# Optimization experiments

Hardware: AMD Instinct MI355X
Metric: run time of the kernel (lower is better)

Reference implementation:

```python
import jax, jax.numpy as jnp
import numpy as np

EMB = 1024
HEADS = 8
SEQ = 4096
LN_EPS = 1e-5


def _layernorm(x, g, b):
    mu = jnp.mean(x, axis=-1, keepdims=True)
    var = jnp.mean(jnp.square(x - mu), axis=-1, keepdims=True)
    return (x - mu) * jax.lax.rsqrt(var + LN_EPS) * g + b


def setup_inputs() -> dict:
    key = jax.random.key(0)
    ks = jax.random.split(key, 12)
    s = 1.0 / np.sqrt(EMB)
    sz = 1.0 / np.sqrt(EMB * HEADS)
    return {
        "history": jax.random.normal(ks[0], (SEQ, EMB), jnp.float32),
        "embdding": jax.random.normal(ks[1], (SEQ, EMB), jnp.float32),
        # per-head Linear weights, torch layout [out, in], stacked over heads
        "Wq_w": jax.random.uniform(ks[2], (HEADS, EMB, EMB), jnp.float32, -s, s),
        "Wq_b": jax.random.uniform(ks[3], (HEADS, EMB), jnp.float32, -s, s),
        "Wk_w": jax.random.uniform(ks[4], (HEADS, EMB, EMB), jnp.float32, -s, s),
        "Wk_b": jax.random.uniform(ks[5], (HEADS, EMB), jnp.float32, -s, s),
        "Wv_w": jax.random.uniform(ks[6], (HEADS, EMB, EMB), jnp.float32, -s, s),
        "Wv_b": jax.random.uniform(ks[7], (HEADS, EMB), jnp.float32, -s, s),
        "Wz_w": jax.random.uniform(ks[8], (EMB, EMB * HEADS), jnp.float32, -sz, sz),
        "Wz_b": jax.random.uniform(ks[9], (EMB,), jnp.float32, -sz, sz),
        "ln1_g": jnp.ones((EMB,), jnp.float32),
        "ln1_b": jnp.zeros((EMB,), jnp.float32),
        "Wf_w": jax.random.uniform(ks[10], (EMB, EMB), jnp.float32, -s, s),
        "Wf_b": jax.random.uniform(ks[11], (EMB,), jnp.float32, -s, s),
        "ln2_g": jnp.ones((EMB,), jnp.float32),
        "ln2_b": jnp.zeros((EMB,), jnp.float32),
    }


def reference(history, embdding, Wq_w, Wq_b, Wk_w, Wk_b, Wv_w, Wv_b,
              Wz_w, Wz_b, ln1_g, ln1_b, Wf_w, Wf_b, ln2_g, ln2_b):
    S, E = embdding.shape
    H = Wq_w.shape[0]
    # per-head linears (torch: y = x @ W.T + b), batched over heads
    Q = jnp.einsum('se,hfe->hsf', embdding, Wq_w) + Wq_b[:, None, :]  # [H,S,E]
    K = jnp.einsum('se,hfe->hsf', embdding, Wk_w) + Wk_b[:, None, :]
    V = jnp.einsum('se,hfe->hsf', history, Wv_w) + Wv_b[:, None, :]
    # K^T @ Q -> [H, E, E], softmax over dim=1 of the 2D matrix == last axis here
    scores = jnp.einsum('hse,hsf->hef', K, Q) / jnp.sqrt(jnp.asarray(E, Q.dtype))
    A = jax.nn.softmax(scores, axis=-1)  # [H,E,E]
    Zh = jnp.einsum('hse,hef->hsf', V, A)  # [H,S,E]
    Z = jnp.transpose(Zh, (1, 0, 2)).reshape(S, H * E)  # cat(dim=1) in head order
    O = Z @ Wz_w.T + Wz_b  # [S,E]
    LN1 = _layernorm(O, ln1_g, ln1_b) + embdding
    FN = LN1 @ Wf_w.T + Wf_b
    LN2 = _layernorm(FN, ln2_g, ln2_b) + LN1
    return LN2
```

## Files before the change

kernel.cpp:

```cpp
#include <hip/hip_runtime.h>


constexpr int EMB = 1024;
constexpr int SEQ = 4096;
constexpr int NH  = 8;

using f32x4  = __attribute__((ext_vector_type(4))) float;
using bf16x8 = __attribute__((ext_vector_type(8))) __bf16;
using us8    = __attribute__((ext_vector_type(8))) unsigned short;
using us4    = __attribute__((ext_vector_type(4))) unsigned short;

#define GLOAD_LDS16(g, l) __builtin_amdgcn_global_load_lds(                 \
    (const __attribute__((address_space(1))) void*)(g),                     \
    (__attribute__((address_space(3))) void*)(l), 16, 0, 0)

__device__ inline unsigned short f2bf(float x) {
  unsigned int u = __float_as_uint(x);
  u += 0x7FFFu + ((u >> 16) & 1u);
  return (unsigned short)(u >> 16);
}
__device__ inline float bf2f(unsigned short h) {
  return __uint_as_float(((unsigned int)h) << 16);
}
__device__ inline f32x4 ntl4(const float* p) {
  return __builtin_nontemporal_load((const f32x4*)p);
}
__device__ inline us4 cvt4(f32x4 x) {
  us4 o; o[0] = f2bf(x[0]); o[1] = f2bf(x[1]); o[2] = f2bf(x[2]); o[3] = f2bf(x[3]);
  return o;
}

template <int MODE>
__device__ __attribute__((always_inline)) void gemm_body(
    unsigned short* lds, int wg,
    const unsigned short* A, const unsigned short* B, void* Cout,
    int K, int lda, int ldb, int ldc,
    long long aZ, long long bZ, long long cZ, int nx, int ny,
    const float* e0, const float* e1, const float* e2, const float* e3,
    float* mpart, float* spart) {
  const int bx = wg % nx;
  const int by = (wg / nx) % ny;
  const int z  = wg / (nx * ny);
  A += (size_t)z * aZ;
  B += (size_t)z * bZ;
  const int tid = threadIdx.x;
  const int lane = tid & 63, wid = tid >> 6;
  const int wm = wid >> 1, wn = wid & 1;
  const int row0 = bx * 64, col0 = by * 128;

  unsigned short* As = lds;
  unsigned short* Bs = lds + 64 * 64;

  f32x4 acc[2][4] = {};
  const int lrow = lane & 15, kg = lane >> 4;
  const int lr = lane >> 3;
  const int lc = (lane & 7) * 8;

  const int nt = K >> 6;
  for (int t = 0; t < nt; ++t) {
    const int k0 = t << 6;
#pragma unroll
    for (int c = 0; c < 2; ++c) {
      int chunk = wid * 2 + c;
      int r = chunk * 8 + lr;
      GLOAD_LDS16(A + (size_t)(row0 + r) * lda + k0 + lc, &As[chunk * 512]);
    }
#pragma unroll
    for (int c = 0; c < 4; ++c) {
      int chunk = wid * 4 + c;
      int r = chunk * 8 + lr;
      GLOAD_LDS16(B + (size_t)(col0 + r) * ldb + k0 + lc, &Bs[chunk * 512]);
    }
    __syncthreads();
#pragma unroll
    for (int ks = 0; ks < 2; ++ks) {
      bf16x8 a[2], b[4];
      int koff = ks * 32 + kg * 8;
#pragma unroll
      for (int i = 0; i < 2; ++i)
        a[i] = *(const bf16x8*)&As[(wm * 32 + i * 16 + lrow) * 64 + koff];
#pragma unroll
      for (int j = 0; j < 4; ++j)
        b[j] = *(const bf16x8*)&Bs[(wn * 64 + j * 16 + lrow) * 64 + koff];
#pragma unroll
      for (int i = 0; i < 2; ++i)
#pragma unroll
        for (int j = 0; j < 4; ++j)
          acc[i][j] = __builtin_amdgcn_mfma_f32_16x16x32_bf16(a[i], b[j], acc[i][j], 0, 0, 0);
    }
    __syncthreads();
  }

  const int rb = (lane >> 4) * 4, cc = lane & 15;
  unsigned short* Cs = lds;
#pragma unroll
  for (int i = 0; i < 2; ++i) {
#pragma unroll
    for (int j = 0; j < 4; ++j) {
#pragma unroll
      for (int r = 0; r < 4; ++r) {
        float val = acc[i][j][r];
        int mm = wm * 32 + i * 16 + rb + r;
        int nn = wn * 64 + j * 16 + cc;
        if (MODE == 4) {
          int m = row0 + mm, n = col0 + nn;
          float bq = e0[z * EMB + m], uu = e1[z * EMB + n];
          float bk = e2[z * EMB + n], vv = e3[z * EMB + m];
          val = (val + bq * (uu + (float)SEQ * bk) + vv * bk) * (1.0f / 32.0f);
        } else if (MODE == 5) {
          val += e0[col0 + nn];
        }
        Cs[mm * 128 + nn] = f2bf(val);
      }
    }
  }
  __syncthreads();
  unsigned short* Cg = (unsigned short*)Cout + (size_t)z * cZ;
#pragma unroll
  for (int p = 0; p < 4; ++p) {
    int idx = p * 256 + tid;
    int row = idx >> 4, col = (idx & 15) * 8;
    *(us8*)(Cg + (size_t)(row0 + row) * ldc + col0 + col) =
        *(const us8*)&Cs[row * 128 + col];
  }
  if (MODE == 4) {
    int colx = tid >> 1, half = tid & 1;
    float mx = -1e30f;
#pragma unroll 8
    for (int r = 0; r < 32; ++r)
      mx = fmaxf(mx, bf2f(Cs[(half * 32 + r) * 128 + colx]));
    mx = fmaxf(mx, __shfl_xor(mx, 1));
    float se = 0.f;
#pragma unroll 8
    for (int r = 0; r < 32; ++r)
      se += __expf(bf2f(Cs[(half * 32 + r) * 128 + colx]) - mx);
    se += __shfl_xor(se, 1);
    if (half == 0) {
      size_t soff = ((size_t)z * 16 + bx) * EMB + col0 + colx;
      mpart[soff] = mx;
      spart[soff] = se;
    }
  }
}

template <int MODE>
__global__ __launch_bounds__(256) void gemm_nt(const unsigned short* __restrict__ A,
                                               const unsigned short* __restrict__ B,
                                               void* __restrict__ Cout,
                                               int K, int lda, int ldb, int ldc,
                                               long long aZ, long long bZ, long long cZ,
                                               int nx, int ny,
                                               const float* __restrict__ e0,
                                               const float* __restrict__ e1,
                                               const float* __restrict__ e2,
                                               const float* __restrict__ e3,
                                               float* __restrict__ mpart,
                                               float* __restrict__ spart) {
  __shared__ __align__(16) unsigned short lds[(64 + 128) * 64];
  const int q = gridDim.x >> 3;
  const int wg = (blockIdx.x & 7) * q + (blockIdx.x >> 3);
  gemm_body<MODE>(lds, wg, A, B, Cout, K, lda, ldb, ldc, aZ, bZ, cZ, nx, ny,
                  e0, e1, e2, e3, mpart, spart);
}

__global__ __launch_bounds__(256) void colsum_xt_k(const float* __restrict__ emb,
                                                   const float* __restrict__ Wv,
                                                   float* __restrict__ part,
                                                   unsigned short* __restrict__ XT,
                                                   unsigned short* __restrict__ WvT) {
  __shared__ float tileT[64][65];
  const int b = blockIdx.x, tid = threadIdx.x;
  if (b < 128) {
    int e = (b & 3) * 256 + tid;
    int y = b >> 2;
    float s = 0.f;
    for (int r = y * 128; r < y * 128 + 128; ++r) s += emb[(size_t)r * EMB + e];
    part[y * EMB + e] = s;
    return;
  }
  const float* src; unsigned short* dst; int R, r0, c0;
  if (b < 1152) {
    int tb = b - 128;
    src = emb; dst = XT; R = SEQ;
    r0 = (tb >> 4) * 64; c0 = (tb & 15) * 64;
  } else {
    int t2 = b - 1152, z = t2 >> 8, tt = t2 & 255;
    src = Wv + (size_t)z * EMB * EMB; dst = WvT + (size_t)z * EMB * EMB;
    R = EMB;
    r0 = (tt >> 4) * 64; c0 = (tt & 15) * 64;
  }
  int tx = tid & 15, ty = tid >> 4;
#pragma unroll
  for (int p = 0; p < 4; ++p) {
    int ir = p * 16 + ty;
    f32x4 x = ntl4(src + (size_t)(r0 + ir) * EMB + c0 + tx * 4);
    tileT[tx * 4 + 0][ir] = x[0]; tileT[tx * 4 + 1][ir] = x[1];
    tileT[tx * 4 + 2][ir] = x[2]; tileT[tx * 4 + 3][ir] = x[3];
  }
  __syncthreads();
#pragma unroll
  for (int p = 0; p < 4; ++p) {
    int orow = p * 16 + ty;
    f32x4 x;
    x[0] = tileT[orow][tx * 4 + 0]; x[1] = tileT[orow][tx * 4 + 1];
    x[2] = tileT[orow][tx * 4 + 2]; x[3] = tileT[orow][tx * 4 + 3];
    *(us4*)(dst + (size_t)(c0 + orow) * R + r0 + tx * 4) = cvt4(x);
  }
}

__global__ __launch_bounds__(256) void colsum_red_k(const float* __restrict__ part,
                                                    float* __restrict__ xbar) {
  int e = blockIdx.x * 256 + threadIdx.x;
  float s = 0.f;
  for (int y = 0; y < 32; ++y) s += part[y * EMB + e];
  xbar[e] = s;
}

__global__ __launch_bounds__(256) void gram_cvt_k(
    const unsigned short* __restrict__ XT, unsigned short* __restrict__ Gp,
    const float* __restrict__ Wk, const float* __restrict__ Wq,
    const float* __restrict__ hist, const float* __restrict__ Wz,
    const float* __restrict__ Wf, const float* __restrict__ xbar,
    unsigned short* __restrict__ Wkb, unsigned short* __restrict__ Wqb,
    unsigned short* __restrict__ Yb, unsigned short* __restrict__ Wzb,
    unsigned short* __restrict__ Wfb,
    float* __restrict__ u, float* __restrict__ v) {
  __shared__ __align__(16) unsigned short smem[(64 + 128) * 64];
  const int tid = threadIdx.x;
  if (blockIdx.x < 1024) {
    const int wg = ((int)blockIdx.x & 7) * 128 + ((int)blockIdx.x >> 3);
    gemm_body<1>(smem, wg, XT, XT, Gp, 512, SEQ, SEQ, EMB,
                 512, 512, (long long)EMB * EMB, 16, 8,
                 nullptr, nullptr, nullptr, nullptr, nullptr, nullptr);
    return;
  }
  int c = blockIdx.x - 1024;
  if (c < 4096) {
    int gw = c * 4 + (tid >> 6);
    int lane = tid & 63;
    const float* src = (gw < 8192) ? Wk : Wq;
    unsigned short* dst = (gw < 8192) ? Wkb : Wqb;
    float* dot = (gw < 8192) ? u : v;
    int row = gw & 8191;
    const float* sr = src + (size_t)row * EMB;
    const float4* xb4 = (const float4*)xbar;
    unsigned short* dr = dst + (size_t)row * EMB;
    float s = 0.f;
#pragma unroll
    for (int j = 0; j < 4; ++j) {
      int idx = j * 64 + lane;
      f32x4 x = ntl4(sr + idx * 4);
      float4 xb = xb4[idx];
      *(us4*)(dr + idx * 4) = cvt4(x);
      s += x[0] * xb.x + x[1] * xb.y + x[2] * xb.z + x[3] * xb.w;
    }
#pragma unroll
    for (int off = 32; off; off >>= 1) s += __shfl_down(s, off);
    if (lane == 0) dot[row] = s;
  } else {
    size_t f0 = (size_t)(c - 4096) * 8192;
    const float* src; unsigned short* dst; size_t loc;
    if (f0 < 4194304ull) { src = hist; dst = Yb; loc = f0; }
    else if (f0 < 12582912ull) { src = Wz; dst = Wzb; loc = f0 - 4194304ull; }
    else { src = Wf; dst = Wfb; loc = f0 - 12582912ull; }
#pragma unroll
    for (int p = 0; p < 8; ++p) {
      int i = p * 256 + tid;
      f32x4 x = ntl4(src + loc + i * 4);
      *(us4*)(dst + loc + i * 4) = cvt4(x);
    }
  }
}

__global__ __launch_bounds__(256) void mp_dvec_k(
    const unsigned short* __restrict__ Cbf, const unsigned short* __restrict__ Wzb,
    unsigned short* __restrict__ Mp,
    const float* __restrict__ bz, const float* __restrict__ cvec,
    float* __restrict__ d) {
  __shared__ __align__(16) unsigned short smem[(64 + 128) * 64];
  const int tid = threadIdx.x;
  if (blockIdx.x < 1024) {
    const int wg = ((int)blockIdx.x & 7) * 128 + ((int)blockIdx.x >> 3);
    gemm_body<1>(smem, wg, Cbf, Wzb, Mp, EMB, EMB, NH * EMB, EMB,
                 (long long)EMB * EMB, (long long)EMB, (long long)EMB * EMB, 16, 8,
                 nullptr, nullptr, nullptr, nullptr, nullptr, nullptr);
    return;
  }
  int g = blockIdx.x - 1024;
  float* sb = (float*)smem;
  const unsigned short* row = Wzb + (size_t)g * (NH * EMB);
  float s = 0.f;
#pragma unroll
  for (int p = 0; p < 4; ++p) {
    int i = p * 256 + tid;
    us8 w = ((const us8*)row)[i];
    float4 c0 = ((const float4*)cvec)[i * 2];
    float4 c1 = ((const float4*)cvec)[i * 2 + 1];
    s += bf2f(w[0]) * c0.x + bf2f(w[1]) * c0.y + bf2f(w[2]) * c0.z + bf2f(w[3]) * c0.w;
    s += bf2f(w[4]) * c1.x + bf2f(w[5]) * c1.y + bf2f(w[6]) * c1.z + bf2f(w[7]) * c1.w;
  }
  int lane = tid & 63, w = tid >> 6;
#pragma unroll
  for (int off = 32; off; off >>= 1) s += __shfl_down(s, off);
  if (lane == 0) sb[w] = s;
  __syncthreads();
  if (tid == 0) d[g] = bz[g] + sb[0] + sb[1] + sb[2] + sb[3];
}

__global__ __launch_bounds__(256) void mred_tr_k(const unsigned short* __restrict__ Mp,
                                                 unsigned short* __restrict__ MT) {
  __shared__ float t[32][33];
  int g0 = blockIdx.x * 32, e0 = blockIdx.y * 32;
  int tx = threadIdx.x & 31, ty = threadIdx.x >> 5;
#pragma unroll
  for (int k = 0; k < 4; ++k) {
    int e = e0 + ty + k * 8;
    float s = 0.f;
#pragma unroll
    for (int h = 0; h < NH; ++h)
      s += bf2f(Mp[((size_t)h << 20) + (size_t)e * EMB + g0 + tx]);
    t[ty + k * 8][tx] = s;
  }
  __syncthreads();
#pragma unroll
  for (int k = 0; k < 4; ++k) {
    int r = ty + k * 8;
    MT[(size_t)(g0 + r) * EMB + e0 + tx] = f2bf(t[tx][r]);
  }
}

__global__ __launch_bounds__(256) void gram_red_k(const unsigned short* __restrict__ Gp,
                                                  unsigned short* __restrict__ Gbf) {
  int i = blockIdx.x * 256 + threadIdx.x;
  float4 s = {0.f, 0.f, 0.f, 0.f};
#pragma unroll
  for (int z = 0; z < 8; ++z) {
    ushort4 v = ((const ushort4*)(Gp + (size_t)z * EMB * EMB))[i];
    s.x += bf2f(v.x); s.y += bf2f(v.y); s.z += bf2f(v.z); s.w += bf2f(v.w);
  }
  ushort4 o; o.x = f2bf(s.x); o.y = f2bf(s.y); o.z = f2bf(s.z); o.w = f2bf(s.w);
  ((ushort4*)Gbf)[i] = o;
}

__global__ __launch_bounds__(256) void colstat2_k(const float* __restrict__ m_part,
                                                  const float* __restrict__ s_part,
                                                  float* __restrict__ mfin,
                                                  float* __restrict__ isfin) {
  int i = blockIdx.x * 256 + threadIdx.x;
  int h = i >> 10, col = i & 1023;
  float M = -1e30f, S = 0.f;
#pragma unroll
  for (int c = 0; c < 16; ++c) {
    float m = m_part[((size_t)h * 16 + c) * EMB + col];
    float s = s_part[((size_t)h * 16 + c) * EMB + col];
    float nm = fmaxf(M, m);
    S = S * __expf(M - nm) + s * __expf(m - nm);
    M = nm;
  }
  mfin[i] = M;
  isfin[i] = 1.0f / S;
}

__global__ __launch_bounds__(256) void at_cvec_k(const unsigned short* __restrict__ ScT,
                                                 const float* __restrict__ mfin,
                                                 const float* __restrict__ isfin,
                                                 const float* __restrict__ bv,
                                                 unsigned short* __restrict__ AT,
                                                 float* __restrict__ cbuf) {
  __shared__ float sb[4];
  int f = blockIdx.x, h = blockIdx.y, tid = threadIdx.x;
  size_t rowoff = ((size_t)h * EMB + f) * EMB;
  ushort4 xr = ((const ushort4*)(ScT + rowoff))[tid];
  float4 m  = ((const float4*)(mfin + (size_t)h * EMB))[tid];
  float4 is = ((const float4*)(isfin + (size_t)h * EMB))[tid];
  float4 b  = ((const float4*)(bv + (size_t)h * EMB))[tid];
  float a0 = __expf(bf2f(xr.x) - m.x) * is.x;
  float a1 = __expf(bf2f(xr.y) - m.y) * is.y;
  float a2 = __expf(bf2f(xr.z) - m.z) * is.z;
  float a3 = __expf(bf2f(xr.w) - m.w) * is.w;
  ushort4 o; o.x = f2bf(a0); o.y = f2bf(a1); o.z = f2bf(a2); o.w = f2bf(a3);
  ((ushort4*)(AT + rowoff))[tid] = o;
  float s = a0 * b.x + a1 * b.y + a2 * b.z + a3 * b.w;
  int lane = tid & 63, w = tid >> 6;
#pragma unroll
  for (int off = 32; off; off >>= 1) s += __shfl_down(s, off);
  if (lane == 0) sb[w] = s;
  __syncthreads();
  if (tid == 0) cbuf[h * EMB + f] = sb[0] + sb[1] + sb[2] + sb[3];
}

__global__ __launch_bounds__(256) void layernorm_k(const unsigned short* __restrict__ Xin,
                                                   const float* __restrict__ resid,
                                                   const float* __restrict__ gw,
                                                   const float* __restrict__ bw,
                                                   float* __restrict__ outf,
                                                   unsigned short* __restrict__ outb) {
  __shared__ float sb[16];
  int row = blockIdx.x, tid = threadIdx.x;
  ushort4 xr = ((const ushort4*)(Xin + (size_t)row * EMB))[tid];
  float v0 = bf2f(xr.x), v1 = bf2f(xr.y), v2 = bf2f(xr.z), v3 = bf2f(xr.w);
  float s = v0 + v1 + v2 + v3;
  float q = v0 * v0 + v1 * v1 + v2 * v2 + v3 * v3;
  int lane = tid & 63, w = tid >> 6;
#pragma unroll
  for (int off = 32; off; off >>= 1) { s += __shfl_down(s, off); q += __shfl_down(q, off); }
  if (lane == 0) { sb[w] = s; sb[8 + w] = q; }
  __syncthreads();
  float mu  = (sb[0] + sb[1] + sb[2] + sb[3]) * (1.0f / EMB);
  float var = (sb[8] + sb[9] + sb[10] + sb[11]) * (1.0f / EMB) - mu * mu;
  float rs = rsqrtf(var + 1e-5f);
  float4 rv = ((const float4*)(resid + (size_t)row * EMB))[tid];
  float4 gv = ((const float4*)gw)[tid];
  float4 bv = ((const float4*)bw)[tid];
  float o0 = (v0 - mu) * rs * gv.x + bv.x + rv.x;
  float o1 = (v1 - mu) * rs * gv.y + bv.y + rv.y;
  float o2 = (v2 - mu) * rs * gv.z + bv.z + rv.z;
  float o3 = (v3 - mu) * rs * gv.w + bv.w + rv.w;
  float4 ov; ov.x = o0; ov.y = o1; ov.z = o2; ov.w = o3;
  ((float4*)(outf + (size_t)row * EMB))[tid] = ov;
  if (outb) {
    ushort4 ob; ob.x = f2bf(o0); ob.y = f2bf(o1); ob.z = f2bf(o2); ob.w = f2bf(o3);
    ((ushort4*)(outb + (size_t)row * EMB))[tid] = ob;
  }
}

extern "C" void kernel_launch(void* const* d_in, const int* in_sizes, int n_in,
                              void* d_out, int out_size, void* d_ws, size_t ws_size,
                              hipStream_t stream) {
  const float* history = (const float*)d_in[0];
  const float* emb     = (const float*)d_in[1];
  const float* Wq_w = (const float*)d_in[2];
  const float* Wq_b = (const float*)d_in[3];
  const float* Wk_w = (const float*)d_in[4];
  const float* Wk_b = (const float*)d_in[5];
  const float* Wv_w = (const float*)d_in[6];
  const float* Wv_b = (const float*)d_in[7];
  const float* Wz_w = (const float*)d_in[8];
  const float* Wz_b = (const float*)d_in[9];
  const float* ln1_g = (const float*)d_in[10];
  const float* ln1_b = (const float*)d_in[11];
  const float* Wf_w = (const float*)d_in[12];
  const float* Wf_b = (const float*)d_in[13];
  const float* ln2_g = (const float*)d_in[14];
  const float* ln2_b = (const float*)d_in[15];

  char* ws = (char*)d_ws;
  const size_t MB = 1024ull * 1024ull;
  unsigned short* XT  = (unsigned short*)(ws + 0);
  unsigned short* Ybf = (unsigned short*)(ws + 8 * MB);
  unsigned short* Wkb = (unsigned short*)(ws + 16 * MB);
  unsigned short* Wqb = (unsigned short*)(ws + 32 * MB);
  unsigned short* WvT = (unsigned short*)(ws + 48 * MB);
  unsigned short* Wzb = (unsigned short*)(ws + 64 * MB);
  unsigned short* Wfb = (unsigned short*)(ws + 80 * MB);
  unsigned short* Gbf = (unsigned short*)(ws + 82 * MB);
  float* xpart = (float*)(ws + 84 * MB);
  float* xbar  = (float*)(ws + 84 * MB + 160 * 1024);
  float* ubuf  = (float*)(ws + 84 * MB + 192 * 1024);
  float* vbuf  = (float*)(ws + 84 * MB + 256 * 1024);
  float* cbuf  = (float*)(ws + 84 * MB + 320 * 1024);
  float* dbuf  = (float*)(ws + 84 * MB + 384 * 1024);
  unsigned short* Tbf = (unsigned short*)(ws + 85 * MB);
  float* Sc  = (float*)(ws + 101 * MB);
  char*  St  = ws + 133 * MB;
  unsigned short* ATb = (unsigned short*)(ws + 149 * MB);
  unsigned short* MTb = (unsigned short*)(ws + 165 * MB);
  float* m_part = (float*)(St);
  float* s_part = (float*)(St + 512 * 1024);
  float* mfin   = (float*)(St + 1024 * 1024);
  float* isfin  = (float*)(St + 1056 * 1024);
  unsigned short* Gp  = (unsigned short*)Sc;
  unsigned short* ScT = (unsigned short*)Sc;
  unsigned short* Cbf = Tbf;
  unsigned short* Mp  = (unsigned short*)Sc;
  unsigned short* Obf = (unsigned short*)St;
  float* LN1  = (float*)ATb;
  unsigned short* LN1b = XT;
  unsigned short* FNbf = Tbf;
  const long long EE = (long long)EMB * EMB;

  colsum_xt_k<<<dim3(3200), 256, 0, stream>>>(emb, Wv_w, xpart, XT, WvT);
  colsum_red_k<<<dim3(4), 256, 0, stream>>>(xpart, xbar);

  gram_cvt_k<<<dim3(6784), 256, 0, stream>>>(XT, Gp,
                                             Wk_w, Wq_w, history, Wz_w, Wf_w,
                                             xbar,
                                             Wkb, Wqb, Ybf, Wzb, Wfb,
                                             ubuf, vbuf);
  gram_red_k<<<dim3(EMB * EMB / 4 / 256), 256, 0, stream>>>(Gp, Gbf);
  gemm_nt<1><<<dim3(1024), 256, 0, stream>>>(Wqb, Gbf, Tbf, EMB, EMB, EMB, EMB,
                                             EE, 0, EE, 16, 8,
                                             nullptr, nullptr, nullptr, nullptr,
                                             nullptr, nullptr);
  gemm_nt<4><<<dim3(1024), 256, 0, stream>>>(Tbf, Wkb, ScT, EMB, EMB, EMB, EMB,
                                             EE, EE, EE, 16, 8,
                                             Wq_b, ubuf, Wk_b, vbuf,
                                             m_part, s_part);
  colstat2_k<<<dim3(32), 256, 0, stream>>>(m_part, s_part, mfin, isfin);
  at_cvec_k<<<dim3(EMB, NH), 256, 0, stream>>>(ScT, mfin, isfin, Wv_b, ATb, cbuf);
  gemm_nt<1><<<dim3(1024), 256, 0, stream>>>(WvT, ATb, Cbf, EMB, EMB, EMB, EMB,
                                             EE, EE, EE, 16, 8,
                                             nullptr, nullptr, nullptr, nullptr,
                                             nullptr, nullptr);
  mp_dvec_k<<<dim3(2048), 256, 0, stream>>>(Cbf, Wzb, Mp, Wz_b, cbuf, dbuf);
  mred_tr_k<<<dim3(EMB / 32, EMB / 32), 256, 0, stream>>>(Mp, MTb);
  gemm_nt<5><<<dim3(512), 256, 0, stream>>>(Ybf, MTb, Obf, EMB, EMB, EMB, EMB,
                                            0, 0, 0, 64, 8,
                                            dbuf, nullptr, nullptr, nullptr,
                                            nullptr, nullptr);
  layernorm_k<<<dim3(SEQ), 256, 0, stream>>>(Obf, emb, ln1_g, ln1_b, LN1, LN1b);
  gemm_nt<5><<<dim3(512), 256, 0, stream>>>(LN1b, Wfb, FNbf, EMB, EMB, EMB, EMB,
                                            0, 0, 0, 64, 8,
                                            Wf_b, nullptr, nullptr, nullptr,
                                            nullptr, nullptr);
  layernorm_k<<<dim3(SEQ), 256, 0, stream>>>(FNbf, LN1, ln2_g, ln2_b, (float*)d_out, nullptr);
}
```

Measured before the change: 273.2 us.

## Exploit Gram matrix symmetry and fold column-stat reduction into softmax kernel

The X^T X Gram GEMM now launches only the upper-triangular 64x128 tiles (576 instead of 1024 workgroups). A new MODE 2 epilogue also writes the transposed tile, so the mirrored half is filled without computing it. Separately, the tiny colstat2 kernel is removed, and each at_cvec block recomputes the online-softmax merge of the 16 partial max/sum values itself. This saves a launch and a round trip at the cost of redundant per-block work and strided transposed LDS reads in the Gram epilogue.

```diff
diff --git a/kernel.cpp b/kernel.cpp
--- a/kernel.cpp
+++ b/kernel.cpp
@@ -32,15 +32,12 @@
 
 template <int MODE>
 __device__ __attribute__((always_inline)) void gemm_body(
-    unsigned short* lds, int wg,
+    unsigned short* lds, int bx, int by, int z,
     const unsigned short* A, const unsigned short* B, void* Cout,
     int K, int lda, int ldb, int ldc,
-    long long aZ, long long bZ, long long cZ, int nx, int ny,
+    long long aZ, long long bZ, long long cZ,
     const float* e0, const float* e1, const float* e2, const float* e3,
     float* mpart, float* spart) {
-  const int bx = wg % nx;
-  const int by = (wg / nx) % ny;
-  const int z  = wg / (nx * ny);
   A += (size_t)z * aZ;
   B += (size_t)z * bZ;
   const int tid = threadIdx.x;
@@ -122,6 +119,18 @@
     int row = idx >> 4, col = (idx & 15) * 8;
     *(us8*)(Cg + (size_t)(row0 + row) * ldc + col0 + col) =
         *(const us8*)&Cs[row * 128 + col];
+  }
+  if (MODE == 2) {
+#pragma unroll
+    for (int p = 0; p < 4; ++p) {
+      int idx = p * 256 + tid;
+      int rr = idx >> 3;
+      int cg = (idx & 7) * 8;
+      us8 o;
+#pragma unroll
+      for (int e = 0; e < 8; ++e) o[e] = Cs[(cg + e) * 128 + rr];
+      *(us8*)(Cg + (size_t)(col0 + rr) * ldc + row0 + cg) = o;
+    }
   }
   if (MODE == 4) {
     int colx = tid >> 1, half = tid & 1;
@@ -159,7 +168,8 @@
   __shared__ __align__(16) unsigned short lds[(64 + 128) * 64];
   const int q = gridDim.x >> 3;
   const int wg = (blockIdx.x & 7) * q + (blockIdx.x >> 3);
-  gemm_body<MODE>(lds, wg, A, B, Cout, K, lda, ldb, ldc, aZ, bZ, cZ, nx, ny,
+  const int bx = wg % nx, by = (wg / nx) % ny, z = wg / (nx * ny);
+  gemm_body<MODE>(lds, bx, by, z, A, B, Cout, K, lda, ldb, ldc, aZ, bZ, cZ,
                   e0, e1, e2, e3, mpart, spart);
 }
 
@@ -227,14 +237,22 @@
     float* __restrict__ u, float* __restrict__ v) {
   __shared__ __align__(16) unsigned short smem[(64 + 128) * 64];
   const int tid = threadIdx.x;
-  if (blockIdx.x < 1024) {
-    const int wg = ((int)blockIdx.x & 7) * 128 + ((int)blockIdx.x >> 3);
-    gemm_body<1>(smem, wg, XT, XT, Gp, 512, SEQ, SEQ, EMB,
-                 512, 512, (long long)EMB * EMB, 16, 8,
+  if (blockIdx.x < 576) {
+    const int wg = ((int)blockIdx.x & 7) * 72 + ((int)blockIdx.x >> 3);
+    const int t = wg % 72, z = wg / 72;
+    int by = 0, st = 0;
+#pragma unroll
+    for (int b = 7; b >= 1; --b) {
+      int sb = 16 * b - b * (b - 1);
+      if (t >= sb && by == 0) { by = b; st = sb; }
+    }
+    int bx = 2 * by + (t - st);
+    gemm_body<2>(smem, bx, by, z, XT, XT, Gp, 512, SEQ, SEQ, EMB,
+                 512, 512, (long long)EMB * EMB,
                  nullptr, nullptr, nullptr, nullptr, nullptr, nullptr);
     return;
   }
-  int c = blockIdx.x - 1024;
+  int c = blockIdx.x - 576;
   if (c < 4096) {
     int gw = c * 4 + (tid >> 6);
     int lane = tid & 63;
@@ -281,8 +299,9 @@
   const int tid = threadIdx.x;
   if (blockIdx.x < 1024) {
     const int wg = ((int)blockIdx.x & 7) * 128 + ((int)blockIdx.x >> 3);
-    gemm_body<1>(smem, wg, Cbf, Wzb, Mp, EMB, EMB, NH * EMB, EMB,
-                 (long long)EMB * EMB, (long long)EMB, (long long)EMB * EMB, 16, 8,
+    const int bx = wg % 16, by = (wg / 16) % 8, z = wg / 128;
+    gemm_body<1>(smem, bx, by, z, Cbf, Wzb, Mp, EMB, EMB, NH * EMB, EMB,
+                 (long long)EMB * EMB, (long long)EMB, (long long)EMB * EMB,
                  nullptr, nullptr, nullptr, nullptr, nullptr, nullptr);
     return;
   }
@@ -342,42 +361,34 @@
   ((ushort4*)Gbf)[i] = o;
 }
 
-__global__ __launch_bounds__(256) void colstat2_k(const float* __restrict__ m_part,
-                                                  const float* __restrict__ s_part,
-                                                  float* __restrict__ mfin,
-                                                  float* __restrict__ isfin) {
-  int i = blockIdx.x * 256 + threadIdx.x;
-  int h = i >> 10, col = i & 1023;
-  float M = -1e30f, S = 0.f;
-#pragma unroll
-  for (int c = 0; c < 16; ++c) {
-    float m = m_part[((size_t)h * 16 + c) * EMB + col];
-    float s = s_part[((size_t)h * 16 + c) * EMB + col];
-    float nm = fmaxf(M, m);
-    S = S * __expf(M - nm) + s * __expf(m - nm);
-    M = nm;
-  }
-  mfin[i] = M;
-  isfin[i] = 1.0f / S;
-}
-
 __global__ __launch_bounds__(256) void at_cvec_k(const unsigned short* __restrict__ ScT,
-                                                 const float* __restrict__ mfin,
-                                                 const float* __restrict__ isfin,
+                                                 const float* __restrict__ m_part,
+                                                 const float* __restrict__ s_part,
                                                  const float* __restrict__ bv,
                                                  unsigned short* __restrict__ AT,
                                                  float* __restrict__ cbuf) {
   __shared__ float sb[4];
   int f = blockIdx.x, h = blockIdx.y, tid = threadIdx.x;
+  f32x4 M; M[0] = M[1] = M[2] = M[3] = -1e30f;
+  f32x4 S; S[0] = S[1] = S[2] = S[3] = 0.f;
+#pragma unroll
+  for (int c = 0; c < 16; ++c) {
+    size_t off = ((size_t)h * 16 + c) * EMB;
+    float4 m4 = ((const float4*)(m_part + off))[tid];
+    float4 s4 = ((const float4*)(s_part + off))[tid];
+    float nm;
+    nm = fmaxf(M[0], m4.x); S[0] = S[0] * __expf(M[0] - nm) + s4.x * __expf(m4.x - nm); M[0] = nm;
+    nm = fmaxf(M[1], m4.y); S[1] = S[1] * __expf(M[1] - nm) + s4.y * __expf(m4.y - nm); M[1] = nm;
+    nm = fmaxf(M[2], m4.z); S[2] = S[2] * __expf(M[2] - nm) + s4.z * __expf(m4.z - nm); M[2] = nm;
+    nm = fmaxf(M[3], m4.w); S[3] = S[3] * __expf(M[3] - nm) + s4.w * __expf(m4.w - nm); M[3] = nm;
+  }
   size_t rowoff = ((size_t)h * EMB + f) * EMB;
   ushort4 xr = ((const ushort4*)(ScT + rowoff))[tid];
-  float4 m  = ((const float4*)(mfin + (size_t)h * EMB))[tid];
-  float4 is = ((const float4*)(isfin + (size_t)h * EMB))[tid];
   float4 b  = ((const float4*)(bv + (size_t)h * EMB))[tid];
-  float a0 = __expf(bf2f(xr.x) - m.x) * is.x;
-  float a1 = __expf(bf2f(xr.y) - m.y) * is.y;
-  float a2 = __expf(bf2f(xr.z) - m.z) * is.z;
-  float a3 = __expf(bf2f(xr.w) - m.w) * is.w;
+  float a0 = __expf(bf2f(xr.x) - M[0]) / S[0];
+  float a1 = __expf(bf2f(xr.y) - M[1]) / S[1];
+  float a2 = __expf(bf2f(xr.z) - M[2]) / S[2];
+  float a3 = __expf(bf2f(xr.w) - M[3]) / S[3];
   ushort4 o; o.x = f2bf(a0); o.y = f2bf(a1); o.z = f2bf(a2); o.w = f2bf(a3);
   ((ushort4*)(AT + rowoff))[tid] = o;
   float s = a0 * b.x + a1 * b.y + a2 * b.z + a3 * b.w;
@@ -467,13 +478,11 @@
   unsigned short* MTb = (unsigned short*)(ws + 165 * MB);
   float* m_part = (float*)(St);
   float* s_part = (float*)(St + 512 * 1024);
-  float* mfin   = (float*)(St + 1024 * 1024);
-  float* isfin  = (float*)(St + 1056 * 1024);
   unsigned short* Gp  = (unsigned short*)Sc;
   unsigned short* ScT = (unsigned short*)Sc;
   unsigned short* Cbf = Tbf;
   unsigned short* Mp  = (unsigned short*)Sc;
-  unsigned short* Obf = (unsigned short*)St;
+  unsigned short* Obf = (unsigned short*)(St + 1024 * 1024);
   float* LN1  = (float*)ATb;
   unsigned short* LN1b = XT;
   unsigned short* FNbf = Tbf;
@@ -482,7 +491,7 @@
   colsum_xt_k<<<dim3(3200), 256, 0, stream>>>(emb, Wv_w, xpart, XT, WvT);
   colsum_red_k<<<dim3(4), 256, 0, stream>>>(xpart, xbar);
 
-  gram_cvt_k<<<dim3(6784), 256, 0, stream>>>(XT, Gp,
+  gram_cvt_k<<<dim3(6336), 256, 0, stream>>>(XT, Gp,
                                              Wk_w, Wq_w, history, Wz_w, Wf_w,
                                              xbar,
                                              Wkb, Wqb, Ybf, Wzb, Wfb,
@@ -496,8 +505,7 @@
                                              EE, EE, EE, 16, 8,
                                              Wq_b, ubuf, Wk_b, vbuf,
                                              m_part, s_part);
-  colstat2_k<<<dim3(32), 256, 0, stream>>>(m_part, s_part, mfin, isfin);
-  at_cvec_k<<<dim3(EMB, NH), 256, 0, stream>>>(ScT, mfin, isfin, Wv_b, ATb, cbuf);
+  at_cvec_k<<<dim3(EMB, NH), 256, 0, stream>>>(ScT, m_part, s_part, Wv_b, ATb, cbuf);
   gemm_nt<1><<<dim3(1024), 256, 0, stream>>>(WvT, ATb, Cbf, EMB, EMB, EMB, EMB,
                                              EE, EE, EE, 16, 8,
                                              nullptr, nullptr, nullptr, nullptr,
```

Result: slower. 303.6 us (+11.1%).
